# Kernel optimization log

Hardware: AMD Instinct MI355X
Metric: run time of the kernel (lower is better)

Reference implementation:

```python
import jax, jax.numpy as jnp
import numpy as np

EPS = 1e-5
N_NODES = 100000
N_EDGES = 1600000
IN_F, HID_F, OUT_F = 128, 128, 64


def setup_inputs() -> dict:
    key = jax.random.key(0)
    ks = jax.random.split(key, 8)
    def xavier(k, fan_in, fan_out):
        lim = float(np.sqrt(6.0 / (fan_in + fan_out)))
        return jax.random.uniform(k, (fan_in, fan_out), jnp.float32, -lim, lim)
    return {
        "features": jax.random.normal(ks[0], (N_NODES, IN_F), jnp.float32),
        "src": jax.random.randint(ks[1], (N_EDGES,), 0, N_NODES, jnp.int64 if jax.config.jax_enable_x64 else jnp.int32),
        "dst": jax.random.randint(ks[2], (N_EDGES,), 0, N_NODES, jnp.int64 if jax.config.jax_enable_x64 else jnp.int32),
        "W_self1": xavier(ks[3], IN_F, HID_F),
        "W_neigh1": xavier(ks[4], IN_F, HID_F),
        "b1": jnp.zeros((HID_F,), jnp.float32),
        "gamma1": jnp.ones((HID_F,), jnp.float32),
        "beta1": jnp.zeros((HID_F,), jnp.float32),
        "W_self2": xavier(ks[5], HID_F, OUT_F),
        "W_neigh2": xavier(ks[6], HID_F, OUT_F),
        "b2": jnp.zeros((OUT_F,), jnp.float32),
        "gamma2": jnp.ones((OUT_F,), jnp.float32),
        "beta2": jnp.zeros((OUT_F,), jnp.float32),
    }


def _sage_conv(h, src, dst, W_self, W_neigh, b, n_nodes):
    # mean aggregation of source-node features onto destination nodes
    agg = jax.ops.segment_sum(h[src], dst, num_segments=n_nodes)   # [N, d]
    deg = jax.ops.segment_sum(jnp.ones_like(dst, dtype=h.dtype), dst, num_segments=n_nodes)
    h_neigh = agg / jnp.maximum(deg, 1.0)[:, None]                  # zero-degree -> 0
    return h @ W_self + h_neigh @ W_neigh + b


def _batchnorm(h, gamma, beta):
    # training-mode BatchNorm1d: batch stats over node dim, biased variance
    mu = jnp.mean(h, axis=0)
    var = jnp.mean(jnp.square(h - mu), axis=0)
    return (h - mu) * jax.lax.rsqrt(var + EPS) * gamma + beta


def reference(features, src, dst, W_self1, W_neigh1, b1, gamma1, beta1,
              W_self2, W_neigh2, b2, gamma2, beta2):
    n = features.shape[0]
    h = _sage_conv(features, src, dst, W_self1, W_neigh1, b1, n)
    h = jax.nn.relu(_batchnorm(h, gamma1, beta1))
    h = _sage_conv(h, src, dst, W_self2, W_neigh2, b2, n)
    return _batchnorm(h, gamma2, beta2)
```

## Files before the change

kernel.cpp:

```cpp
#include <hip/hip_runtime.h>

#define EPS_BN 1e-5f
#define BINSHIFT 9
#define BINW 512
#define P_EPB 8192
#define LDS_CAP 10240
#define NREP 32

typedef __attribute__((ext_vector_type(8))) short short8;
typedef __attribute__((ext_vector_type(4))) float f32x4;

__device__ __forceinline__ unsigned short f2bf(float x) {
    unsigned int u = __float_as_uint(x);
    u += 0x7fffu + ((u >> 16) & 1u);
    return (unsigned short)(u >> 16);
}
__device__ __forceinline__ float bf2f(unsigned short h) {
    return __uint_as_float(((unsigned int)h) << 16);
}
__device__ __forceinline__ float bflo(unsigned u) { return __uint_as_float(u << 16); }
__device__ __forceinline__ float bfhi(unsigned u) { return __uint_as_float(u & 0xffff0000u); }
__device__ __forceinline__ float i8lo(unsigned short u) { return (float)(signed char)(u & 0xff); }
__device__ __forceinline__ float i8hi(unsigned short u) { return (float)(signed char)(u >> 8); }

__device__ __forceinline__ void scan512(int* a, int t) {
    for (int off = 1; off < 512; off <<= 1) {
        int v = (t >= off) ? a[t - off] : 0;
        __syncthreads();
        a[t] += v;
        __syncthreads();
    }
}
__device__ __forceinline__ void scan256(int* a, int t) {
    for (int off = 1; off < 256; off <<= 1) {
        int v = (t >= off) ? a[t - off] : 0;
        __syncthreads();
        a[t] += v;
        __syncthreads();
    }
}

__global__ __launch_bounds__(256) void prep_kernel(
    const float* __restrict__ Ws1, const float* __restrict__ Wn1,
    const float* __restrict__ Ws2, const float* __restrict__ Wn2,
    unsigned short* __restrict__ W1f, unsigned short* __restrict__ W2f,
    const int* __restrict__ dst, int* __restrict__ counts, int E, int NB, int wB) {
    int tid = threadIdx.x;
    if (blockIdx.x < wB) {
        int i = blockIdx.x * 256 + tid;
        if (i < 128 * 256) {
            int j = i & 7, L = (i >> 3) & 63, c = (i >> 9) & 15, kk = i >> 13;
            int k = kk * 32 + (L >> 4) * 8 + j;
            int col = c * 16 + (L & 15);
            float v = (col < 128) ? Ws1[k * 128 + col] : Wn1[k * 128 + (col - 128)];
            W1f[i] = f2bf(v);
        } else {
            int idx = i - 128 * 256;
            if (idx < 128 * 128) {
                int j = idx & 7, L = (idx >> 3) & 63, c = (idx >> 9) & 7, kk = idx >> 12;
                int k = kk * 32 + (L >> 4) * 8 + j;
                int col = c * 16 + (L & 15);
                float v = (col < 64) ? Ws2[k * 64 + col] : Wn2[k * 64 + (col - 64)];
                W2f[idx] = f2bf(v);
            }
        }
    } else {
        __shared__ int hist[512];
        int blk = blockIdx.x - wB;
        int e0 = blk * P_EPB, e1 = min(e0 + P_EPB, E);
        for (int b = tid; b < 512; b += 256) hist[b] = 0;
        __syncthreads();
        for (int e = e0 + tid; e < e1; e += 256) atomicAdd(&hist[dst[e] >> BINSHIFT], 1);
        __syncthreads();
        for (int b = tid; b < NB; b += 256) counts[blk * NB + b] = hist[b];
    }
}

__global__ __launch_bounds__(256) void p2a(const int* __restrict__ counts,
                                           int* __restrict__ segrel,
                                           int* __restrict__ tot, int NB, int NBLK) {
    __shared__ int s[256];
    int b = blockIdx.x, t = threadIdx.x;
    int v = (t < NBLK) ? counts[t * NB + b] : 0;
    s[t] = v;
    __syncthreads();
    scan256(s, t);
    if (t < NBLK) segrel[t * NB + b] = s[t] - v;
    if (t == 255) tot[b] = s[255];
}

__global__ __launch_bounds__(512) void p3_scatter(const int* __restrict__ src,
                                                  const int* __restrict__ dst,
                                                  const int* __restrict__ segrel,
                                                  const int* __restrict__ tot,
                                                  unsigned* __restrict__ epack,
                                                  int E, int NB) {
    __shared__ unsigned lp[P_EPB];
    __shared__ int hist[512];
    __shared__ int sBase[513];
    __shared__ int cursor[512];
    __shared__ int bbase[512];
    int t = threadIdx.x;
    int blk = blockIdx.x;
    int e0 = blk * P_EPB, e1 = min(e0 + P_EPB, E), m = e1 - e0;
    int tv = (t < NB) ? tot[t] : 0;
    bbase[t] = tv;
    __syncthreads();
    scan512(bbase, t);
    bbase[t] -= tv;
    hist[t] = 0;
    __syncthreads();
    for (int e = e0 + t; e < e1; e += 512) atomicAdd(&hist[dst[e] >> BINSHIFT], 1);
    __syncthreads();
    int h = hist[t];
    scan512(hist, t);
    int excl = hist[t] - h;
    sBase[t] = excl;
    cursor[t] = excl;
    if (t == 0) sBase[512] = m;
    __syncthreads();
    for (int e = e0 + t; e < e1; e += 512) {
        int d = dst[e];
        int pos = atomicAdd(&cursor[d >> BINSHIFT], 1);
        lp[pos] = ((unsigned)src[e] << BINSHIFT) | ((unsigned)d & (BINW - 1));
    }
    __syncthreads();
    for (int i = t; i < m; i += 512) {
        int lo = 0, hi = NB;
        while (hi - lo > 1) {
            int mid = (lo + hi) >> 1;
            if (sBase[mid] <= i) lo = mid; else hi = mid;
        }
        epack[bbase[lo] + segrel[blk * NB + lo] + (i - sBase[lo])] = lp[i];
    }
}

__global__ __launch_bounds__(512) void p4_csr(const unsigned* __restrict__ epack,
                                              const int* __restrict__ tot,
                                              int* __restrict__ row_start,
                                              int* __restrict__ cntg,
                                              float* __restrict__ inv_deg,
                                              int* __restrict__ csr_src, int N, int NB) {
    __shared__ int ncnt[512];
    __shared__ int cursor[512];
    __shared__ int bb[512];
    __shared__ int lsrc[LDS_CAP];
    int t = threadIdx.x;
    int b = blockIdx.x;
    int tv = (t < NB) ? tot[t] : 0;
    bb[t] = tv;
    __syncthreads();
    scan512(bb, t);
    int e1 = bb[b];
    int e0 = bb[b] - tot[b];
    int m = e1 - e0;
    int nbase = b << BINSHIFT;
    int nn = min(N - nbase, BINW);
    ncnt[t] = 0;
    __syncthreads();
    for (int i = e0 + t; i < e1; i += 512)
        atomicAdd(&ncnt[epack[i] & (BINW - 1)], 1);
    __syncthreads();
    int c = ncnt[t];
    scan512(ncnt, t);
    int excl = ncnt[t] - c;
    if (t < nn) {
        int node = nbase + t;
        row_start[node] = e0 + excl;
        cntg[node] = c;
        inv_deg[node] = 1.0f / fmaxf((float)c, 1.0f);
    }
    cursor[t] = excl;
    __syncthreads();
    for (int i = e0 + t; i < e1; i += 512) {
        unsigned v = epack[i];
        int pos = atomicAdd(&cursor[v & (BINW - 1)], 1);
        if (pos < LDS_CAP) lsrc[pos] = (int)(v >> BINSHIFT);
    }
    __syncthreads();
    int mm = min(m, LDS_CAP);
    for (int i = t; i < mm; i += 512) csr_src[e0 + i] = lsrc[i];
}

template <int MT, int MSELF, bool SELFBF, bool FUSEBN, bool AFP32>
__global__ __launch_bounds__(256) void gemm_dual(const unsigned short* __restrict__ Ab,
                                                 const float* __restrict__ Af,
                                                 const unsigned short* __restrict__ Wf,
                                                 float* __restrict__ YselfF,
                                                 unsigned short* __restrict__ YselfB,
                                                 signed char* __restrict__ Ynb8,
                                                 float* __restrict__ scl, int N,
                                                 const float* __restrict__ sums,
                                                 const float* __restrict__ gamma,
                                                 const float* __restrict__ beta,
                                                 float invN) {
    constexpr int K = 128;
    constexpr int NCT = MT / 16;
    constexpr int NCTW = NCT / 2;
    constexpr int KS = K / 32;
    constexpr int MNB = MT - MSELF;
    static_assert(MSELF * 2 == MT, "col-half split requires MSELF == MT/2");
    __shared__ float ssc[128], ssh[128];

    if constexpr (FUSEBN) {
        if (threadIdx.x < 128) {
            int c = threadIdx.x;
            float su = 0.f, sq = 0.f;
            for (int r = 0; r < NREP; r++) {
                su += sums[r * 256 + c];
                sq += sums[r * 256 + 128 + c];
            }
            float mu = su * invN;
            float var = sq * invN - mu * mu;
            float sc = gamma[c] * rsqrtf(var + EPS_BN);
            ssc[c] = sc;
            ssh[c] = beta[c] - mu * sc;
        }
        __syncthreads();
    }

    int wv = threadIdx.x >> 6, lane = threadIdx.x & 63;
    int ch = wv & 1;
    int rt = wv >> 1;
    int row0 = blockIdx.x * 64 + rt * 32;
    int m = lane & 15, quad = lane >> 4;

    short8 afrag[2][KS];
#pragma unroll
    for (int t = 0; t < 2; t++) {
        int arow = row0 + t * 16 + m;
        if (arow >= N) arow = N - 1;
#pragma unroll
        for (int kk = 0; kk < KS; kk++) {
            short8 raw;
            if (AFP32) {
                const float* ap = Af + (size_t)arow * K + quad * 8 + kk * 32;
                f32x4 a = *(const f32x4*)ap;
                f32x4 b = *(const f32x4*)(ap + 4);
#pragma unroll
                for (int j = 0; j < 4; j++) {
                    raw[j] = (short)f2bf(a[j]);
                    raw[4 + j] = (short)f2bf(b[j]);
                }
            } else {
                raw = *(const short8*)(Ab + (size_t)arow * K + quad * 8 + kk * 32);
            }
            if (FUSEBN) {
#pragma unroll
                for (int j = 0; j < 8; j++) {
                    int c = kk * 32 + quad * 8 + j;
                    float f = bf2f((unsigned short)raw[j]) * ssc[c] + ssh[c];
                    raw[j] = (short)f2bf(fmaxf(f, 0.f));
                }
            }
            afrag[t][kk] = raw;
        }
    }

    f32x4 acc[2][NCTW];
#pragma unroll
    for (int t = 0; t < 2; t++)
        for (int ci = 0; ci < NCTW; ci++)
            for (int j = 0; j < 4; j++) acc[t][ci][j] = 0.f;

    const short8* Bf = (const short8*)Wf;
    int cbase = ch * NCTW;
#pragma unroll
    for (int kk = 0; kk < KS; kk++) {
#pragma unroll
        for (int ci = 0; ci < NCTW; ci++) {
            short8 bfrag = Bf[(kk * NCT + cbase + ci) * 64 + lane];
#pragma unroll
            for (int t = 0; t < 2; t++)
                acc[t][ci] = __builtin_amdgcn_mfma_f32_16x16x32_bf16(afrag[t][kk], bfrag,
                                                                     acc[t][ci], 0, 0, 0);
        }
    }

    if (ch == 0) {
#pragma unroll
        for (int t = 0; t < 2; t++) {
#pragma unroll
            for (int ci = 0; ci < NCTW; ci++) {
                int colg = ci * 16 + m;
#pragma unroll
                for (int r = 0; r < 4; r++) {
                    int row = row0 + t * 16 + quad * 4 + r;
                    if (row < N) {
                        float v = acc[t][ci][r];
                        if (SELFBF)
                            YselfB[(size_t)row * MSELF + colg] = f2bf(v);
                        else
                            YselfF[(size_t)row * MSELF + colg] = v;
                    }
                }
            }
        }
    } else {
#pragma unroll
        for (int t = 0; t < 2; t++) {
#pragma unroll
            for (int r = 0; r < 4; r++) {
                float mx = 0.f;
#pragma unroll
                for (int ci = 0; ci < NCTW; ci++) mx = fmaxf(mx, fabsf(acc[t][ci][r]));
#pragma unroll
                for (int off = 1; off < 16; off <<= 1) mx = fmaxf(mx, __shfl_xor(mx, off));
                int row = row0 + t * 16 + quad * 4 + r;
                float qs = 127.0f / fmaxf(mx, 1e-30f);
                if (row < N) {
                    if (m == 0) scl[row] = mx * (1.0f / 127.0f);
#pragma unroll
                    for (int ci = 0; ci < NCTW; ci++) {
                        int colg = ci * 16 + m;
                        int q = __float2int_rn(acc[t][ci][r] * qs);
                        Ynb8[(size_t)row * MNB + colg] = (signed char)q;
                    }
                }
            }
        }
    }
}

__global__ __launch_bounds__(256) void agg_row128(const unsigned int* __restrict__ Sb,
                                                  const unsigned short* __restrict__ Tq,
                                                  const float* __restrict__ scl,
                                                  const int* __restrict__ row_start,
                                                  const int* __restrict__ cnt,
                                                  const float* __restrict__ inv_deg,
                                                  const int* __restrict__ csr_src,
                                                  const float* __restrict__ bias,
                                                  unsigned int* __restrict__ Out,
                                                  float* __restrict__ sums,
                                                  int N, int totalWaves) {
    int wv = threadIdx.x >> 6, lane = threadIdx.x & 63;
    int c = lane * 2;
    float bs0 = bias[c], bs1 = bias[c + 1];
    float S0 = 0.f, S1 = 0.f, Q0 = 0.f, Q1 = 0.f;

    int n = blockIdx.x * 4 + wv;
    int pStart = 0, pEc = 0, pIv = 0;
    float pInv = 0.f;
    if (n < N) {
        pStart = row_start[n];
        pEc = cnt[n];
        pInv = inv_deg[n];
        if (pEc > 0) pIv = csr_src[pStart + min(lane, min(pEc, 64) - 1)];
    }
    for (; n < N; n += totalWaves) {
        int start = pStart, ec = pEc, iv = pIv;
        float inv = pInv;
        unsigned su = Sb[(size_t)n * 64 + lane];
        int n2 = n + totalWaves;
        if (n2 < N) {
            pStart = row_start[n2];
            pEc = cnt[n2];
            pInv = inv_deg[n2];
            if (pEc > 0) pIv = csr_src[pStart + min(lane, min(pEc, 64) - 1)];
        }
        float a0 = 0.f, a1 = 0.f;
        for (int base = 0; base < ec; base += 64) {
            int ecc = min(ec - base, 64);
            if (base) iv = csr_src[start + base + min(lane, ecc - 1)];
            int e = 0;
            for (; e + 16 <= ecc; e += 16) {
                unsigned short u[16];
                float sc[16];
#pragma unroll
                for (int j = 0; j < 16; j++) {
                    int s = __builtin_amdgcn_readlane(iv, e + j);
                    u[j] = Tq[(size_t)s * 64 + lane];
                    sc[j] = scl[s];
                }
#pragma unroll
                for (int j = 0; j < 16; j++) {
                    a0 += sc[j] * i8lo(u[j]);
                    a1 += sc[j] * i8hi(u[j]);
                }
            }
            if (e + 8 <= ecc) {
                unsigned short u[8];
                float sc[8];
#pragma unroll
                for (int j = 0; j < 8; j++) {
                    int s = __builtin_amdgcn_readlane(iv, e + j);
                    u[j] = Tq[(size_t)s * 64 + lane];
                    sc[j] = scl[s];
                }
#pragma unroll
                for (int j = 0; j < 8; j++) {
                    a0 += sc[j] * i8lo(u[j]);
                    a1 += sc[j] * i8hi(u[j]);
                }
                e += 8;
            }
            if (e < ecc) {
                int r = ecc - e;
                unsigned short u[8];
                float sc[8];
#pragma unroll
                for (int j = 0; j < 8; j++) {
                    int s = __builtin_amdgcn_readlane(iv, min(e + j, ecc - 1));
                    u[j] = Tq[(size_t)s * 64 + lane];
                    sc[j] = scl[s];
                }
#pragma unroll
                for (int j = 0; j < 8; j++) {
                    if (j < r) {
                        a0 += sc[j] * i8lo(u[j]);
                        a1 += sc[j] * i8hi(u[j]);
                    }
                }
            }
        }
        float h0 = bflo(su) + a0 * inv + bs0;
        float h1 = bfhi(su) + a1 * inv + bs1;
        Out[(size_t)n * 64 + lane] = (unsigned)f2bf(h0) | ((unsigned)f2bf(h1) << 16);
        S0 += h0; Q0 += h0 * h0;
        S1 += h1; Q1 += h1 * h1;
    }
    __shared__ float ls[256];
    ls[threadIdx.x] = 0.f;
    __syncthreads();
    atomicAdd(&ls[c], S0);
    atomicAdd(&ls[c + 1], S1);
    atomicAdd(&ls[128 + c], Q0);
    atomicAdd(&ls[129 + c], Q1);
    __syncthreads();
    float* dstS = sums + (size_t)(blockIdx.x & (NREP - 1)) * 256;
    atomicAdd(&dstS[threadIdx.x], ls[threadIdx.x]);
}

__global__ __launch_bounds__(256) void agg_row64(const unsigned short* __restrict__ Tq,
                                                 const float* __restrict__ scl,
                                                 const int* __restrict__ row_start,
                                                 const int* __restrict__ cnt,
                                                 const float* __restrict__ inv_deg,
                                                 const int* __restrict__ csr_src,
                                                 const float* __restrict__ bias,
                                                 float* Self, float* __restrict__ sums,
                                                 int N, int totalWaves) {
    int wv = threadIdx.x >> 6, lane = threadIdx.x & 63;
    int g = lane >> 5, h = lane & 31;
    int c = h * 2;
    float bs0 = bias[c], bs1 = bias[c + 1];
    float S0 = 0.f, S1 = 0.f, Q0 = 0.f, Q1 = 0.f;

    int n = blockIdx.x * 4 + wv;
    int pStart = 0, pEc = 0, pIv = 0;
    if (n < N) {
        pStart = row_start[n];
        pEc = cnt[n];
        if (pEc > 0) pIv = csr_src[pStart + min(lane, min(pEc, 64) - 1)];
    }
    for (; n < N; n += totalWaves) {
        int start = pStart, ec = pEc, iv = pIv;
        float inv = inv_deg[n];
        int n2 = n + totalWaves;
        if (n2 < N) {
            pStart = row_start[n2];
            pEc = cnt[n2];
            if (pEc > 0) pIv = csr_src[pStart + min(lane, min(pEc, 64) - 1)];
        }
        float a0 = 0.f, a1 = 0.f;
        for (int base = 0; base < ec; base += 64) {
            int ecc = min(ec - base, 64);
            if (base) iv = csr_src[start + base + min(lane, ecc - 1)];
            int e = 0;
            for (; e + 8 <= ecc; e += 8) {
                unsigned short u[4];
                float sc[4];
#pragma unroll
                for (int j = 0; j < 4; j++) {
                    int s0 = __builtin_amdgcn_readlane(iv, e + 2 * j);
                    int s1 = __builtin_amdgcn_readlane(iv, e + 2 * j + 1);
                    int sg = g ? s1 : s0;
                    u[j] = Tq[(size_t)sg * 32 + h];
                    sc[j] = scl[sg];
                }
#pragma unroll
                for (int j = 0; j < 4; j++) {
                    a0 += sc[j] * i8lo(u[j]);
                    a1 += sc[j] * i8hi(u[j]);
                }
            }
            if (e < ecc) {
                int r = ecc - e;
                unsigned short u[4];
                float sc[4];
#pragma unroll
                for (int j = 0; j < 4; j++) {
                    int s0 = __builtin_amdgcn_readlane(iv, min(e + 2 * j, ecc - 1));
                    int s1 = __builtin_amdgcn_readlane(iv, min(e + 2 * j + 1, ecc - 1));
                    int sg = g ? s1 : s0;
                    u[j] = Tq[(size_t)sg * 32 + h];
                    sc[j] = scl[sg];
                }
#pragma unroll
                for (int j = 0; j < 4; j++) {
                    bool ok = (2 * j + g) < r;
                    a0 += ok ? sc[j] * i8lo(u[j]) : 0.f;
                    a1 += ok ? sc[j] * i8hi(u[j]) : 0.f;
                }
            }
        }
        a0 += __shfl_xor(a0, 32);
        a1 += __shfl_xor(a1, 32);
        if (g == 0) {
            size_t off = (size_t)n * 64 + c;
            float h0 = Self[off] + a0 * inv + bs0;
            float h1 = Self[off + 1] + a1 * inv + bs1;
            Self[off] = h0;
            Self[off + 1] = h1;
            S0 += h0; Q0 += h0 * h0;
            S1 += h1; Q1 += h1 * h1;
        }
    }
    __shared__ float ls[128];
    if (threadIdx.x < 128) ls[threadIdx.x] = 0.f;
    __syncthreads();
    if (g == 0) {
        atomicAdd(&ls[c], S0);
        atomicAdd(&ls[c + 1], S1);
        atomicAdd(&ls[64 + c], Q0);
        atomicAdd(&ls[65 + c], Q1);
    }
    __syncthreads();
    if (threadIdx.x < 128) {
        float* dstS = sums + (size_t)(blockIdx.x & (NREP - 1)) * 128;
        atomicAdd(&dstS[threadIdx.x], ls[threadIdx.x]);
    }
}

__global__ __launch_bounds__(256) void bn_apply_f64(float* H, const float* __restrict__ sums,
                                                    const float* __restrict__ gamma,
                                                    const float* __restrict__ beta,
                                                    int N, float invN) {
    __shared__ float ss[128];
    int tid = threadIdx.x;
    if (tid < 64) {
        float su = 0.f, sq = 0.f;
        for (int r = 0; r < NREP; r++) {
            su += sums[r * 128 + tid];
            sq += sums[r * 128 + 64 + tid];
        }
        float mu = su * invN;
        float var = sq * invN - mu * mu;
        float sc = gamma[tid] * rsqrtf(var + EPS_BN);
        ss[tid] = sc;
        ss[64 + tid] = beta[tid] - mu * sc;
    }
    __syncthreads();
    int total4 = N * 16;
    float4* H4 = (float4*)H;
    for (int i = blockIdx.x * 256 + threadIdx.x; i < total4; i += 256 * gridDim.x) {
        int c0 = (i * 4) & 63;
        float4 v = H4[i];
        float4 sc = *(const float4*)&ss[c0];
        float4 sh = *(const float4*)&ss[64 + c0];
        v.x = v.x * sc.x + sh.x;
        v.y = v.y * sc.y + sh.y;
        v.z = v.z * sc.z + sh.z;
        v.w = v.w * sc.w + sh.w;
        H4[i] = v;
    }
}

extern "C" void kernel_launch(void* const* d_in, const int* in_sizes, int n_in,
                              void* d_out, int out_size, void* d_ws, size_t ws_size,
                              hipStream_t stream) {
    const float* X = (const float*)d_in[0];
    const int* src = (const int*)d_in[1];
    const int* dst = (const int*)d_in[2];
    const float* Wself1 = (const float*)d_in[3];
    const float* Wneigh1 = (const float*)d_in[4];
    const float* b1 = (const float*)d_in[5];
    const float* g1 = (const float*)d_in[6];
    const float* be1 = (const float*)d_in[7];
    const float* Wself2 = (const float*)d_in[8];
    const float* Wneigh2 = (const float*)d_in[9];
    const float* b2 = (const float*)d_in[10];
    const float* g2 = (const float*)d_in[11];
    const float* be2 = (const float*)d_in[12];
    float* out = (float*)d_out;

    const int N = in_sizes[0] / 128;
    const int E = in_sizes[1];
    const int NB = (N + BINW - 1) >> BINSHIFT;
    const int NBLK = (E + P_EPB - 1) / P_EPB;

    char* p = (char*)d_ws;
    auto carve = [&](size_t bytes) {
        char* r = p;
        p += (bytes + 255) & ~(size_t)255;
        return r;
    };
    float* sums1 = (float*)carve((size_t)NREP * 256 * 4);
    float* sums2 = (float*)carve((size_t)NREP * 128 * 4);
    size_t zero_bytes = (size_t)(p - (char*)d_ws);
    int* counts = (int*)carve((size_t)NBLK * NB * 4);
    int* segrel = (int*)carve((size_t)NBLK * NB * 4);
    int* tot = (int*)carve((size_t)NB * 4);
    unsigned* epack = (unsigned*)carve((size_t)E * 4);
    int* csr_src = (int*)carve((size_t)E * 4);
    int* row_start = (int*)carve((size_t)N * 4);
    int* cntg = (int*)carve((size_t)N * 4);
    float* inv_deg = (float*)carve((size_t)N * 4);
    unsigned short* W1f = (unsigned short*)carve(128 * 256 * 2);
    unsigned short* W2f = (unsigned short*)carve(128 * 128 * 2);
    unsigned short* bufS = (unsigned short*)carve((size_t)N * 128 * 2);
    signed char* Tq1 = (signed char*)carve((size_t)N * 128);
    float* scl1 = (float*)carve((size_t)N * 4);
    signed char* Tq2 = (signed char*)carve((size_t)N * 64);
    float* scl2 = (float*)carve((size_t)N * 4);
    unsigned short* h1b = (unsigned short*)carve((size_t)N * 128 * 2);

    hipMemsetAsync(d_ws, 0, zero_bytes, stream);

    const int wB = 192;
    const float invN = 1.0f / (float)N;
    prep_kernel<<<wB + NBLK, 256, 0, stream>>>(Wself1, Wneigh1, Wself2, Wneigh2, W1f, W2f,
                                               dst, counts, E, NB, wB);
    p2a<<<NB, 256, 0, stream>>>(counts, segrel, tot, NB, NBLK);
    p3_scatter<<<NBLK, 512, 0, stream>>>(src, dst, segrel, tot, epack, E, NB);
    p4_csr<<<NB, 512, 0, stream>>>(epack, tot, row_start, cntg, inv_deg, csr_src, N, NB);

    int ggrid = (N + 63) / 64;
    gemm_dual<256, 128, true, false, true><<<ggrid, 256, 0, stream>>>(
        nullptr, X, W1f, nullptr, bufS, Tq1, scl1, N, nullptr, nullptr, nullptr, 0.f);
    agg_row128<<<2048, 256, 0, stream>>>(
        (const unsigned int*)bufS, (const unsigned short*)Tq1, scl1, row_start, cntg,
        inv_deg, csr_src, b1, (unsigned int*)h1b, sums1, N, 8192);

    gemm_dual<128, 64, false, true, false><<<ggrid, 256, 0, stream>>>(
        h1b, nullptr, W2f, out, nullptr, Tq2, scl2, N, sums1, g1, be1, invN);
    agg_row64<<<2048, 256, 0, stream>>>(
        (const unsigned short*)Tq2, scl2, row_start, cntg, inv_deg, csr_src, b2, out,
        sums2, N, 8192);
    bn_apply_f64<<<2048, 256, 0, stream>>>(out, sums2, g2, be2, N, invN);
}
```

Before: 338.3 us.

## Scatter edges directly, stage GEMM A tiles in LDS, add dynamic work queues

The edge scatter kernel drops its LDS local sort and binary-search copy-out. Each edge now claims a global position through per-bin LDS cursors seeded from segment offsets and writes straight to epack. The dual GEMM first stages the 64-row A tile into padded LDS with coalesced loads, then reads fragments from there. Both aggregation kernels swap static strided node assignment for atomic work queues over 8 partitions, handing out 4 nodes per grab, to balance skewed degrees. The trade-offs are uncoalesced scatter writes, extra LDS use that may cut GEMM occupancy, and added atomic traffic.

```diff
diff --git a/kernel.cpp b/kernel.cpp
--- a/kernel.cpp
+++ b/kernel.cpp
@@ -95,43 +95,22 @@
                                                   const int* __restrict__ tot,
                                                   unsigned* __restrict__ epack,
                                                   int E, int NB) {
-    __shared__ unsigned lp[P_EPB];
-    __shared__ int hist[512];
-    __shared__ int sBase[513];
-    __shared__ int cursor[512];
-    __shared__ int bbase[512];
+    __shared__ int cur[512];
     int t = threadIdx.x;
     int blk = blockIdx.x;
-    int e0 = blk * P_EPB, e1 = min(e0 + P_EPB, E), m = e1 - e0;
+    int e0 = blk * P_EPB, e1 = min(e0 + P_EPB, E);
     int tv = (t < NB) ? tot[t] : 0;
-    bbase[t] = tv;
-    __syncthreads();
-    scan512(bbase, t);
-    bbase[t] -= tv;
-    hist[t] = 0;
-    __syncthreads();
-    for (int e = e0 + t; e < e1; e += 512) atomicAdd(&hist[dst[e] >> BINSHIFT], 1);
-    __syncthreads();
-    int h = hist[t];
-    scan512(hist, t);
-    int excl = hist[t] - h;
-    sBase[t] = excl;
-    cursor[t] = excl;
-    if (t == 0) sBase[512] = m;
+    cur[t] = tv;
+    __syncthreads();
+    scan512(cur, t);
+    int base = cur[t] - tv;
+    __syncthreads();
+    cur[t] = (t < NB) ? (base + segrel[blk * NB + t]) : 0;
     __syncthreads();
     for (int e = e0 + t; e < e1; e += 512) {
         int d = dst[e];
-        int pos = atomicAdd(&cursor[d >> BINSHIFT], 1);
-        lp[pos] = ((unsigned)src[e] << BINSHIFT) | ((unsigned)d & (BINW - 1));
-    }
-    __syncthreads();
-    for (int i = t; i < m; i += 512) {
-        int lo = 0, hi = NB;
-        while (hi - lo > 1) {
-            int mid = (lo + hi) >> 1;
-            if (sBase[mid] <= i) lo = mid; else hi = mid;
-        }
-        epack[bbase[lo] + segrel[blk * NB + lo] + (i - sBase[lo])] = lp[i];
+        int pos = atomicAdd(&cur[d >> BINSHIFT], 1);
+        epack[pos] = ((unsigned)src[e] << BINSHIFT) | ((unsigned)d & (BINW - 1));
     }
 }
 
@@ -199,8 +178,11 @@
     constexpr int NCTW = NCT / 2;
     constexpr int KS = K / 32;
     constexpr int MNB = MT - MSELF;
+    constexpr int APADF = 132;
+    constexpr int APADH = 136;
     static_assert(MSELF * 2 == MT, "col-half split requires MSELF == MT/2");
     __shared__ float ssc[128], ssh[128];
+    __shared__ __align__(16) char AsRaw[AFP32 ? (64 * APADF * 4) : (64 * APADH * 2)];
 
     if constexpr (FUSEBN) {
         if (threadIdx.x < 128) {
@@ -216,25 +198,43 @@
             ssc[c] = sc;
             ssh[c] = beta[c] - mu * sc;
         }
-        __syncthreads();
-    }
+    }
+
+    int row0g = blockIdx.x * 64;
+    if (AFP32) {
+        float* As = (float*)AsRaw;
+        for (int i = threadIdx.x; i < 64 * 32; i += 256) {
+            int r = i >> 5, cv = i & 31;
+            int gr = row0g + r;
+            if (gr >= N) gr = N - 1;
+            *(f32x4*)&As[r * APADF + cv * 4] = *(const f32x4*)&Af[(size_t)gr * K + cv * 4];
+        }
+    } else {
+        unsigned short* As = (unsigned short*)AsRaw;
+        for (int i = threadIdx.x; i < 64 * 16; i += 256) {
+            int r = i >> 4, cv = i & 15;
+            int gr = row0g + r;
+            if (gr >= N) gr = N - 1;
+            *(short8*)&As[r * APADH + cv * 8] = *(const short8*)&Ab[(size_t)gr * K + cv * 8];
+        }
+    }
+    __syncthreads();
 
     int wv = threadIdx.x >> 6, lane = threadIdx.x & 63;
     int ch = wv & 1;
     int rt = wv >> 1;
-    int row0 = blockIdx.x * 64 + rt * 32;
+    int row0 = row0g + rt * 32;
     int m = lane & 15, quad = lane >> 4;
 
     short8 afrag[2][KS];
 #pragma unroll
     for (int t = 0; t < 2; t++) {
-        int arow = row0 + t * 16 + m;
-        if (arow >= N) arow = N - 1;
+        int lr = rt * 32 + t * 16 + m;
 #pragma unroll
         for (int kk = 0; kk < KS; kk++) {
             short8 raw;
             if (AFP32) {
-                const float* ap = Af + (size_t)arow * K + quad * 8 + kk * 32;
+                const float* ap = ((const float*)AsRaw) + lr * APADF + quad * 8 + kk * 32;
                 f32x4 a = *(const f32x4*)ap;
                 f32x4 b = *(const f32x4*)(ap + 4);
 #pragma unroll
@@ -243,7 +243,8 @@
                     raw[4 + j] = (short)f2bf(b[j]);
                 }
             } else {
-                raw = *(const short8*)(Ab + (size_t)arow * K + quad * 8 + kk * 32);
+                raw = *(const short8*)(((const unsigned short*)AsRaw) + lr * APADH +
+                                       quad * 8 + kk * 32);
             }
             if (FUSEBN) {
 #pragma unroll
@@ -332,92 +333,97 @@
                                                   const float* __restrict__ bias,
                                                   unsigned int* __restrict__ Out,
                                                   float* __restrict__ sums,
-                                                  int N, int totalWaves) {
+                                                  int N, int* __restrict__ wq) {
     int wv = threadIdx.x >> 6, lane = threadIdx.x & 63;
     int c = lane * 2;
     float bs0 = bias[c], bs1 = bias[c + 1];
     float S0 = 0.f, S1 = 0.f, Q0 = 0.f, Q1 = 0.f;
-
-    int n = blockIdx.x * 4 + wv;
-    int pStart = 0, pEc = 0, pIv = 0;
-    float pInv = 0.f;
-    if (n < N) {
-        pStart = row_start[n];
-        pEc = cnt[n];
-        pInv = inv_deg[n];
+    int part = blockIdx.x & 7;
+    int p0 = (int)(((long)N * part) >> 3);
+    int p1 = (int)(((long)N * (part + 1)) >> 3);
+    (void)wv;
+
+    for (;;) {
+        int t0 = 0;
+        if (lane == 0) t0 = atomicAdd(&wq[part], 4);
+        int nb = p0 + __shfl(t0, 0);
+        if (nb >= p1) break;
+        int ne = min(nb + 4, p1);
+        int pStart = row_start[nb], pEc = cnt[nb];
+        float pInv = inv_deg[nb];
+        int pIv = 0;
         if (pEc > 0) pIv = csr_src[pStart + min(lane, min(pEc, 64) - 1)];
-    }
-    for (; n < N; n += totalWaves) {
-        int start = pStart, ec = pEc, iv = pIv;
-        float inv = pInv;
-        unsigned su = Sb[(size_t)n * 64 + lane];
-        int n2 = n + totalWaves;
-        if (n2 < N) {
-            pStart = row_start[n2];
-            pEc = cnt[n2];
-            pInv = inv_deg[n2];
-            if (pEc > 0) pIv = csr_src[pStart + min(lane, min(pEc, 64) - 1)];
-        }
-        float a0 = 0.f, a1 = 0.f;
-        for (int base = 0; base < ec; base += 64) {
-            int ecc = min(ec - base, 64);
-            if (base) iv = csr_src[start + base + min(lane, ecc - 1)];
-            int e = 0;
-            for (; e + 16 <= ecc; e += 16) {
-                unsigned short u[16];
-                float sc[16];
-#pragma unroll
-                for (int j = 0; j < 16; j++) {
-                    int s = __builtin_amdgcn_readlane(iv, e + j);
-                    u[j] = Tq[(size_t)s * 64 + lane];
-                    sc[j] = scl[s];
-                }
-#pragma unroll
-                for (int j = 0; j < 16; j++) {
-                    a0 += sc[j] * i8lo(u[j]);
-                    a1 += sc[j] * i8hi(u[j]);
-                }
-            }
-            if (e + 8 <= ecc) {
-                unsigned short u[8];
-                float sc[8];
-#pragma unroll
-                for (int j = 0; j < 8; j++) {
-                    int s = __builtin_amdgcn_readlane(iv, e + j);
-                    u[j] = Tq[(size_t)s * 64 + lane];
-                    sc[j] = scl[s];
-                }
-#pragma unroll
-                for (int j = 0; j < 8; j++) {
-                    a0 += sc[j] * i8lo(u[j]);
-                    a1 += sc[j] * i8hi(u[j]);
-                }
-                e += 8;
-            }
-            if (e < ecc) {
-                int r = ecc - e;
-                unsigned short u[8];
-                float sc[8];
-#pragma unroll
-                for (int j = 0; j < 8; j++) {
-                    int s = __builtin_amdgcn_readlane(iv, min(e + j, ecc - 1));
-                    u[j] = Tq[(size_t)s * 64 + lane];
-                    sc[j] = scl[s];
-                }
-#pragma unroll
-                for (int j = 0; j < 8; j++) {
-                    if (j < r) {
+        for (int n = nb; n < ne; n++) {
+            int start = pStart, ec = pEc, iv = pIv;
+            float inv = pInv;
+            unsigned su = Sb[(size_t)n * 64 + lane];
+            if (n + 1 < ne) {
+                pStart = row_start[n + 1];
+                pEc = cnt[n + 1];
+                pInv = inv_deg[n + 1];
+                if (pEc > 0) pIv = csr_src[pStart + min(lane, min(pEc, 64) - 1)];
+            }
+            float a0 = 0.f, a1 = 0.f;
+            for (int base = 0; base < ec; base += 64) {
+                int ecc = min(ec - base, 64);
+                if (base) iv = csr_src[start + base + min(lane, ecc - 1)];
+                int e = 0;
+                for (; e + 16 <= ecc; e += 16) {
+                    unsigned short u[16];
+                    float sc[16];
+#pragma unroll
+                    for (int j = 0; j < 16; j++) {
+                        int s = __builtin_amdgcn_readlane(iv, e + j);
+                        u[j] = Tq[(unsigned)s * 64u + (unsigned)lane];
+                        sc[j] = scl[s];
+                    }
+#pragma unroll
+                    for (int j = 0; j < 16; j++) {
                         a0 += sc[j] * i8lo(u[j]);
                         a1 += sc[j] * i8hi(u[j]);
                     }
                 }
-            }
-        }
-        float h0 = bflo(su) + a0 * inv + bs0;
-        float h1 = bfhi(su) + a1 * inv + bs1;
-        Out[(size_t)n * 64 + lane] = (unsigned)f2bf(h0) | ((unsigned)f2bf(h1) << 16);
-        S0 += h0; Q0 += h0 * h0;
-        S1 += h1; Q1 += h1 * h1;
+                if (e + 8 <= ecc) {
+                    unsigned short u[8];
+                    float sc[8];
+#pragma unroll
+                    for (int j = 0; j < 8; j++) {
+                        int s = __builtin_amdgcn_readlane(iv, e + j);
+                        u[j] = Tq[(unsigned)s * 64u + (unsigned)lane];
+                        sc[j] = scl[s];
+                    }
+#pragma unroll
+                    for (int j = 0; j < 8; j++) {
+                        a0 += sc[j] * i8lo(u[j]);
+                        a1 += sc[j] * i8hi(u[j]);
+                    }
+                    e += 8;
+                }
+                if (e < ecc) {
+                    int r = ecc - e;
+                    unsigned short u[8];
+                    float sc[8];
+#pragma unroll
+                    for (int j = 0; j < 8; j++) {
+                        int s = __builtin_amdgcn_readlane(iv, min(e + j, ecc - 1));
+                        u[j] = Tq[(unsigned)s * 64u + (unsigned)lane];
+                        sc[j] = scl[s];
+                    }
+#pragma unroll
+                    for (int j = 0; j < 8; j++) {
+                        if (j < r) {
+                            a0 += sc[j] * i8lo(u[j]);
+                            a1 += sc[j] * i8hi(u[j]);
+                        }
+                    }
+                }
+            }
+            float h0 = bflo(su) + a0 * inv + bs0;
+            float h1 = bfhi(su) + a1 * inv + bs1;
+            Out[(size_t)n * 64 + lane] = (unsigned)f2bf(h0) | ((unsigned)f2bf(h1) << 16);
+            S0 += h0; Q0 += h0 * h0;
+            S1 += h1; Q1 += h1 * h1;
+        }
     }
     __shared__ float ls[256];
     ls[threadIdx.x] = 0.f;
@@ -439,81 +445,87 @@
                                                  const int* __restrict__ csr_src,
                                                  const float* __restrict__ bias,
                                                  float* Self, float* __restrict__ sums,
-                                                 int N, int totalWaves) {
+                                                 int N, int* __restrict__ wq) {
     int wv = threadIdx.x >> 6, lane = threadIdx.x & 63;
     int g = lane >> 5, h = lane & 31;
     int c = h * 2;
     float bs0 = bias[c], bs1 = bias[c + 1];
     float S0 = 0.f, S1 = 0.f, Q0 = 0.f, Q1 = 0.f;
-
-    int n = blockIdx.x * 4 + wv;
-    int pStart = 0, pEc = 0, pIv = 0;
-    if (n < N) {
-        pStart = row_start[n];
-        pEc = cnt[n];
+    int part = blockIdx.x & 7;
+    int p0 = (int)(((long)N * part) >> 3);
+    int p1 = (int)(((long)N * (part + 1)) >> 3);
+    (void)wv;
+
+    for (;;) {
+        int t0 = 0;
+        if (lane == 0) t0 = atomicAdd(&wq[part], 4);
+        int nb = p0 + __shfl(t0, 0);
+        if (nb >= p1) break;
+        int ne = min(nb + 4, p1);
+        int pStart = row_start[nb], pEc = cnt[nb];
+        int pIv = 0;
         if (pEc > 0) pIv = csr_src[pStart + min(lane, min(pEc, 64) - 1)];
-    }
-    for (; n < N; n += totalWaves) {
-        int start = pStart, ec = pEc, iv = pIv;
-        float inv = inv_deg[n];
-        int n2 = n + totalWaves;
-        if (n2 < N) {
-            pStart = row_start[n2];
-            pEc = cnt[n2];
-            if (pEc > 0) pIv = csr_src[pStart + min(lane, min(pEc, 64) - 1)];
-        }
-        float a0 = 0.f, a1 = 0.f;
-        for (int base = 0; base < ec; base += 64) {
-            int ecc = min(ec - base, 64);
-            if (base) iv = csr_src[start + base + min(lane, ecc - 1)];
-            int e = 0;
-            for (; e + 8 <= ecc; e += 8) {
-                unsigned short u[4];
-                float sc[4];
-#pragma unroll
-                for (int j = 0; j < 4; j++) {
-                    int s0 = __builtin_amdgcn_readlane(iv, e + 2 * j);
-                    int s1 = __builtin_amdgcn_readlane(iv, e + 2 * j + 1);
-                    int sg = g ? s1 : s0;
-                    u[j] = Tq[(size_t)sg * 32 + h];
-                    sc[j] = scl[sg];
-                }
-#pragma unroll
-                for (int j = 0; j < 4; j++) {
-                    a0 += sc[j] * i8lo(u[j]);
-                    a1 += sc[j] * i8hi(u[j]);
-                }
-            }
-            if (e < ecc) {
-                int r = ecc - e;
-                unsigned short u[4];
-                float sc[4];
-#pragma unroll
-                for (int j = 0; j < 4; j++) {
-                    int s0 = __builtin_amdgcn_readlane(iv, min(e + 2 * j, ecc - 1));
-                    int s1 = __builtin_amdgcn_readlane(iv, min(e + 2 * j + 1, ecc - 1));
-                    int sg = g ? s1 : s0;
-                    u[j] = Tq[(size_t)sg * 32 + h];
-                    sc[j] = scl[sg];
-                }
-#pragma unroll
-                for (int j = 0; j < 4; j++) {
-                    bool ok = (2 * j + g) < r;
-                    a0 += ok ? sc[j] * i8lo(u[j]) : 0.f;
-                    a1 += ok ? sc[j] * i8hi(u[j]) : 0.f;
-                }
-            }
-        }
-        a0 += __shfl_xor(a0, 32);
-        a1 += __shfl_xor(a1, 32);
-        if (g == 0) {
-            size_t off = (size_t)n * 64 + c;
-            float h0 = Self[off] + a0 * inv + bs0;
-            float h1 = Self[off + 1] + a1 * inv + bs1;
-            Self[off] = h0;
-            Self[off + 1] = h1;
-            S0 += h0; Q0 += h0 * h0;
-            S1 += h1; Q1 += h1 * h1;
+        for (int n = nb; n < ne; n++) {
+            int start = pStart, ec = pEc, iv = pIv;
+            float inv = inv_deg[n];
+            if (n + 1 < ne) {
+                pStart = row_start[n + 1];
+                pEc = cnt[n + 1];
+                if (pEc > 0) pIv = csr_src[pStart + min(lane, min(pEc, 64) - 1)];
+            }
+            float a0 = 0.f, a1 = 0.f;
+            for (int base = 0; base < ec; base += 64) {
+                int ecc = min(ec - base, 64);
+                if (base) iv = csr_src[start + base + min(lane, ecc - 1)];
+                int e = 0;
+                for (; e + 8 <= ecc; e += 8) {
+                    unsigned short u[4];
+                    float sc[4];
+#pragma unroll
+                    for (int j = 0; j < 4; j++) {
+                        int s0 = __builtin_amdgcn_readlane(iv, e + 2 * j);
+                        int s1 = __builtin_amdgcn_readlane(iv, e + 2 * j + 1);
+                        int sg = g ? s1 : s0;
+                        u[j] = Tq[(unsigned)sg * 32u + (unsigned)h];
+                        sc[j] = scl[sg];
+                    }
+#pragma unroll
+                    for (int j = 0; j < 4; j++) {
+                        a0 += sc[j] * i8lo(u[j]);
+                        a1 += sc[j] * i8hi(u[j]);
+                    }
+                }
+                if (e < ecc) {
+                    int r = ecc - e;
+                    unsigned short u[4];
+                    float sc[4];
+#pragma unroll
+                    for (int j = 0; j < 4; j++) {
+                        int s0 = __builtin_amdgcn_readlane(iv, min(e + 2 * j, ecc - 1));
+                        int s1 = __builtin_amdgcn_readlane(iv, min(e + 2 * j + 1, ecc - 1));
+                        int sg = g ? s1 : s0;
+                        u[j] = Tq[(unsigned)sg * 32u + (unsigned)h];
+                        sc[j] = scl[sg];
+                    }
+#pragma unroll
+                    for (int j = 0; j < 4; j++) {
+                        bool ok = (2 * j + g) < r;
+                        a0 += ok ? sc[j] * i8lo(u[j]) : 0.f;
+                        a1 += ok ? sc[j] * i8hi(u[j]) : 0.f;
+                    }
+                }
+            }
+            a0 += __shfl_xor(a0, 32);
+            a1 += __shfl_xor(a1, 32);
+            if (g == 0) {
+                size_t off = (size_t)n * 64 + c;
+                float h0 = Self[off] + a0 * inv + bs0;
+                float h1 = Self[off + 1] + a1 * inv + bs1;
+                Self[off] = h0;
+                Self[off + 1] = h1;
+                S0 += h0; Q0 += h0 * h0;
+                S1 += h1; Q1 += h1 * h1;
+            }
         }
     }
     __shared__ float ls[128];
@@ -597,6 +609,8 @@
     };
     float* sums1 = (float*)carve((size_t)NREP * 256 * 4);
     float* sums2 = (float*)carve((size_t)NREP * 128 * 4);
+    int* wq1 = (int*)carve(8 * 4);
+    int* wq2 = (int*)carve(8 * 4);
     size_t zero_bytes = (size_t)(p - (char*)d_ws);
     int* counts = (int*)carve((size_t)NBLK * NB * 4);
     int* segrel = (int*)carve((size_t)NBLK * NB * 4);
@@ -630,12 +644,12 @@
         nullptr, X, W1f, nullptr, bufS, Tq1, scl1, N, nullptr, nullptr, nullptr, 0.f);
     agg_row128<<<2048, 256, 0, stream>>>(
         (const unsigned int*)bufS, (const unsigned short*)Tq1, scl1, row_start, cntg,
-        inv_deg, csr_src, b1, (unsigned int*)h1b, sums1, N, 8192);
+        inv_deg, csr_src, b1, (unsigned int*)h1b, sums1, N, wq1);
 
     gemm_dual<128, 64, false, true, false><<<ggrid, 256, 0, stream>>>(
         h1b, nullptr, W2f, out, nullptr, Tq2, scl2, N, sums1, g1, be1, invN);
     agg_row64<<<2048, 256, 0, stream>>>(
         (const unsigned short*)Tq2, scl2, row_start, cntg, inv_deg, csr_src, b2, out,
-        sums2, N, 8192);
+        sums2, N, wq2);
     bn_apply_f64<<<2048, 256, 0, stream>>>(out, sums2, g2, be2, N, invN);
 }
```

Result: slower. 985.2 us (+191.2%).
